# Optimization experiments

Hardware: AMD Instinct MI355X
Metric: run time of the kernel (lower is better)

## Reference

```python
import jax, jax.numpy as jnp
import numpy as np

PAD_TOKEN = -2.0
EPS = 1e-6
NEG_INF = -1.0e9


def _layer_norm(x, gamma, beta):
    mu = jnp.mean(x, axis=-1, keepdims=True)
    var = jnp.mean(jnp.square(x - mu), axis=-1, keepdims=True)
    return (x - mu) * jax.lax.rsqrt(var + EPS) * gamma + beta


def setup_inputs() -> dict:
    key = jax.random.key(0)
    ks = jax.random.split(key, 10)
    B, N, M, D, H, E, O = 128, 32, 384, 256, 8, 32, 256
    S = N + M
    x_pmhc = jax.random.normal(ks[0], (B, S, D), jnp.float32)
    # masks hold raw token values; PAD_TOKEN marks padding positions
    p_len = jax.random.randint(ks[1], (B,), 8, N + 1)
    m_len = jax.random.randint(ks[2], (B,), M // 2, M + 1)
    p_mask = jnp.where(jnp.arange(N)[None, :] < p_len[:, None], 1.0, PAD_TOKEN).astype(jnp.float32)
    m_mask = jnp.where(jnp.arange(M)[None, :] < m_len[:, None], 1.0, PAD_TOKEN).astype(jnp.float32)
    # learned params (keras random_normal init stddev=0.05; random_uniform in [-0.05, 0.05])
    q_proj = 0.05 * jax.random.normal(ks[3], (H, D, E), jnp.float32)
    k_proj = 0.05 * jax.random.normal(ks[4], (H, D, E), jnp.float32)
    v_proj = 0.05 * jax.random.normal(ks[5], (H, D, E), jnp.float32)
    g_proj = jax.random.uniform(ks[6], (H, D, E), jnp.float32, -0.05, 0.05)
    out_w = 0.05 * jax.random.normal(ks[7], (H * E, O), jnp.float32)
    out_b = jnp.zeros((O,), jnp.float32)
    ln1_g = jnp.ones((D,), jnp.float32)
    ln1_b = jnp.zeros((D,), jnp.float32)
    ln2_g = jnp.ones((O,), jnp.float32)
    ln2_b = jnp.zeros((O,), jnp.float32)
    return dict(x_pmhc=x_pmhc, p_mask=p_mask, m_mask=m_mask,
                q_proj=q_proj, k_proj=k_proj, v_proj=v_proj, g_proj=g_proj,
                out_w=out_w, out_b=out_b,
                ln1_g=ln1_g, ln1_b=ln1_b, ln2_g=ln2_g, ln2_b=ln2_b)


def _mask_2d(p, m):
    # p: [B,N] in {0,1}, m: [B,M] in {0,1}
    B, N = p.shape
    M = m.shape[1]
    cross_pm = p[:, :, None] * m[:, None, :]          # [B,N,M]
    cross_mp = m[:, :, None] * p[:, None, :]          # [B,M,N]
    top = jnp.concatenate([jnp.zeros((B, N, N), p.dtype), cross_pm], axis=2)
    bot = jnp.concatenate([cross_mp, jnp.zeros((B, M, M), p.dtype)], axis=2)
    return jnp.concatenate([top, bot], axis=1)        # [B,S,S]


def reference(x_pmhc, p_mask, m_mask, q_proj, k_proj, v_proj, g_proj,
              out_w, out_b, ln1_g, ln1_b, ln2_g, ln2_b):
    H, _, E = q_proj.shape
    B, S, _ = x_pmhc.shape
    scale = 1.0 / jnp.sqrt(jnp.asarray(E, jnp.float32))
    x = _layer_norm(x_pmhc, ln1_g, ln1_b)
    p = jnp.where(p_mask == PAD_TOKEN, 0.0, 1.0)
    m = jnp.where(m_mask == PAD_TOKEN, 0.0, 1.0)
    q = jnp.einsum('bxd,hde->bhxe', x, q_proj)
    k = jnp.einsum('bxd,hde->bhxe', x, k_proj)
    v = jnp.einsum('bxd,hde->bhxe', x, v_proj)
    g = jnp.einsum('bxd,hde->bhxe', x, g_proj)
    att = jnp.einsum('bhxe,bhye->bhxy', q, k) * scale          # [B,H,S,S]
    mask2d = _mask_2d(p, m)                                     # [B,S,S]
    att = jax.nn.softmax(att + ((1.0 - mask2d) * NEG_INF)[:, None], axis=-1)
    att = att * mask2d[:, None]
    out = jnp.einsum('bhxy,bhye->bhxe', att, v)
    out = out * jax.nn.sigmoid(g)
    out = out.transpose(0, 2, 1, 3).reshape(B, S, H * E)
    out = out @ out_w + out_b
    return _layer_norm(out, ln2_g, ln2_b)
```

## Files before the change

kernel.cpp:

```cpp
#include <hip/hip_runtime.h>

typedef unsigned short u16;
typedef __bf16 bf16x8 __attribute__((ext_vector_type(8)));
typedef float f32x4 __attribute__((ext_vector_type(4)));

#define B_    128
#define S_    416
#define NPEP  32
#define MMHC  384
#define D_    256
#define H_    8
#define E_    32
#define O_    256
#define BS_   (B_ * S_)

#define PAD_TOK (-2.0f)
#define SCALE_E 0.17677669529663687f

typedef const __attribute__((address_space(1))) void cg_void;
typedef __attribute__((address_space(3))) void lds_void;

__device__ __forceinline__ float bf2f(u16 u) {
  union { unsigned int i; float f; } x; x.i = ((unsigned int)u) << 16; return x.f;
}
__device__ __forceinline__ u16 f2bf(float f) {
  union { float f; unsigned int i; } x; x.f = f;
  unsigned int i = x.i;
  return (u16)((i + 0x7FFFu + ((i >> 16) & 1u)) >> 16);
}
__device__ __forceinline__ unsigned pk2bf(float lo, float hi) {
  return (unsigned)f2bf(lo) | ((unsigned)f2bf(hi) << 16);
}

__global__ __launch_bounds__(256)
void prep(const float* __restrict__ q, const float* __restrict__ k,
          const float* __restrict__ v, const float* __restrict__ g,
          const float* __restrict__ ow, u16* __restrict__ WT, u16* __restrict__ WoT,
          const float* __restrict__ x, u16* __restrict__ xln,
          const float* __restrict__ gam, const float* __restrict__ bet) {
  const int bx = blockIdx.x, t = threadIdx.x;
  if (bx < 1024) {
    const int col = bx;
    const int p = col >> 8, h = (col >> 5) & 7, e = col & 31;
    const float* src = (p == 0) ? q : (p == 1) ? k : (p == 2) ? v : g;
    WT[col * 256 + t] = f2bf(src[(h * 256 + t) * 32 + e]);
    return;
  }
  if (bx < 1280) {
    const int n = bx - 1024;
    WoT[n * 256 + t] = f2bf(ow[t * 256 + n]);
    return;
  }
  const int w = t >> 6, lane = t & 63;
  const size_t row = (size_t)(bx - 1280) * 4 + w;
  const float4 u = *((const float4*)x + row * 64 + lane);
  const float x0 = u.x, x1 = u.y, x2 = u.z, x3 = u.w;
  float sum = (x0 + x1) + (x2 + x3);
  float ss  = (x0 * x0 + x1 * x1) + (x2 * x2 + x3 * x3);
  #pragma unroll
  for (int off = 32; off; off >>= 1) {
    sum += __shfl_xor(sum, off);
    ss  += __shfl_xor(ss, off);
  }
  const float mean = sum * 0.00390625f;
  float var = ss * 0.00390625f - mean * mean;
  var = fmaxf(var, 0.0f);
  const float rs = rsqrtf(var + 1e-6f);
  const float4 g4 = *((const float4*)gam + lane);
  const float4 b4 = *((const float4*)bet + lane);
  ushort4 r;
  r.x = f2bf((x0 - mean) * rs * g4.x + b4.x);
  r.y = f2bf((x1 - mean) * rs * g4.y + b4.y);
  r.z = f2bf((x2 - mean) * rs * g4.z + b4.z);
  r.w = f2bf((x3 - mean) * rs * g4.w + b4.w);
  *((ushort4*)xln + row * 64 + lane) = r;
}

__global__ __launch_bounds__(256, 4)
void gemm_qkvg(const u16* __restrict__ A, const u16* __restrict__ BT,
               u16* __restrict__ Qh, u16* __restrict__ Kh,
               u16* __restrict__ Vh, u16* __restrict__ Gh) {
  __shared__ __attribute__((aligned(16))) u16 As[128 * 64];
  __shared__ __attribute__((aligned(16))) u16 Bs[128 * 64];
  const int L = blockIdx.x;
  const int m0 = ((L & 7) + 8 * (L >> 6)) * 128;
  const int n0 = ((L >> 3) & 7) * 128;
  const int tid = threadIdx.x;
  const int lane = tid & 63;
  const int w = tid >> 6;
  const int wr = (w >> 1) * 64;
  const int wc = (w & 1) * 64;
  const int mi = lane & 15;
  const int quad = lane >> 4;
  const int rseg = lane >> 3;
  const int gcol = (lane & 7) ^ rseg;
  f32x4 acc[4][4] = {};
  for (int kc = 0; kc < 256; kc += 64) {
    __syncthreads();
    #pragma unroll
    for (int j = 0; j < 4; ++j) {
      const int seg = w * 4 + j;
      const int r = seg * 8 + rseg;
      const u16* ga = &A[(size_t)(m0 + r) * 256 + kc + gcol * 8];
      __builtin_amdgcn_global_load_lds((cg_void*)ga, (lds_void*)&As[seg * 512], 16, 0, 0);
      const u16* gb = &BT[(size_t)(n0 + r) * 256 + kc + gcol * 8];
      __builtin_amdgcn_global_load_lds((cg_void*)gb, (lds_void*)&Bs[seg * 512], 16, 0, 0);
    }
    __syncthreads();
    #pragma unroll
    for (int kt = 0; kt < 2; ++kt) {
      bf16x8 a[4], bb[4];
      #pragma unroll
      for (int i = 0; i < 4; ++i) {
        const int m = wr + i * 16 + mi;
        const int pg = (kt * 4 + quad) ^ (mi & 7);
        a[i] = *(const bf16x8*)&As[m * 64 + pg * 8];
      }
      #pragma unroll
      for (int i = 0; i < 4; ++i) {
        const int n = wc + i * 16 + mi;
        const int pg = (kt * 4 + quad) ^ (mi & 7);
        bb[i] = *(const bf16x8*)&Bs[n * 64 + pg * 8];
      }
      #pragma unroll
      for (int i = 0; i < 4; ++i)
        #pragma unroll
        for (int jn = 0; jn < 4; ++jn)
          acc[i][jn] = __builtin_amdgcn_mfma_f32_16x16x32_bf16(a[i], bb[jn], acc[i][jn], 0, 0, 0);
    }
  }
  u16* dstj[4];
  #pragma unroll
  for (int jn = 0; jn < 4; ++jn) {
    const int colb = n0 + wc + jn * 16;
    const int p = colb >> 8;
    const int h = (colb >> 5) & 7;
    const int e = (colb & 16) + mi;
    u16* bp = (p == 0) ? Qh : (p == 1) ? Kh : (p == 2) ? Vh : Gh;
    dstj[jn] = bp + (size_t)h * BS_ * 32 + e;
  }
  #pragma unroll
  for (int i = 0; i < 4; ++i) {
    const int row = m0 + wr + i * 16 + quad * 4;
    #pragma unroll
    for (int r = 0; r < 4; ++r) {
      #pragma unroll
      for (int jn = 0; jn < 4; ++jn)
        dstj[jn][(size_t)(row + r) * 32] = f2bf(acc[i][jn][r]);
    }
  }
}

__global__ __launch_bounds__(256, 4)
void att_fused(const u16* __restrict__ Qh, const u16* __restrict__ Kh,
               const u16* __restrict__ Vh, const u16* __restrict__ Gh,
               const float* __restrict__ p_mask, const float* __restrict__ m_mask,
               u16* __restrict__ atto) {
  __shared__ __attribute__((aligned(16))) u16 VT[32][392];
  __shared__ __attribute__((aligned(16))) u16 VpT[32][40];
  __shared__ __attribute__((aligned(16))) float pf[32];
  __shared__ __attribute__((aligned(16))) float mfl[384];
  const int bh = blockIdx.x;
  const int b = bh >> 3, h = bh & 7;
  const int t = threadIdx.x;
  const int lane = t & 63, w = t >> 6;
  const int mi = lane & 15, quad = lane >> 4;
  const size_t hb = (size_t)h * BS_ + (size_t)b * S_;

  if (t < 32) pf[t] = (p_mask[b * NPEP + t] == PAD_TOK) ? 0.0f : 1.0f;
  mfl[t] = (m_mask[b * MMHC + t] == PAD_TOK) ? 0.0f : 1.0f;
  if (t < 128) mfl[256 + t] = (m_mask[b * MMHC + 256 + t] == PAD_TOK) ? 0.0f : 1.0f;
  {
    const int y = t >> 3, e0 = (t & 7) * 4;
    const ushort4 u = *(const ushort4*)&Vh[(hb + y) * 32 + e0];
    VpT[e0 + 0][y] = u.x; VpT[e0 + 1][y] = u.y;
    VpT[e0 + 2][y] = u.z; VpT[e0 + 3][y] = u.w;
  }
  #pragma unroll
  for (int i = 0; i < 12; ++i) {
    const int idx = i * 256 + t;
    const int y = idx >> 3, e0 = (idx & 7) * 4;
    const ushort4 u = *(const ushort4*)&Vh[(hb + 32 + y) * 32 + e0];
    VT[e0 + 0][y] = u.x; VT[e0 + 1][y] = u.y;
    VT[e0 + 2][y] = u.z; VT[e0 + 3][y] = u.w;
  }
  __syncthreads();

  const f32x4 fz = {0.0f, 0.0f, 0.0f, 0.0f};
  const int idxA = ((quad & 1) * 2) * 16 + mi;
  const int idxB = idxA + 16;
  const bool hi = quad >= 2;
  union U8 { unsigned u[4]; bf16x8 v; };

  if (w < 2) {
    const bf16x8 aq = *(const bf16x8*)&Qh[(hb + w * 16 + mi) * 32 + quad * 8];
    float lsum = 0.0f;
    f32x4 o0 = fz, o1 = fz;
    #pragma unroll
    for (int ks = 0; ks < 12; ++ks) {
      unsigned pA0, pA1, pB0, pB1;
      {
        const int kt = 2 * ks;
        const bf16x8 bk = *(const bf16x8*)&Kh[(hb + 32 + kt * 16 + mi) * 32 + quad * 8];
        const f32x4 s = __builtin_amdgcn_mfma_f32_16x16x32_bf16(bk, aq, fz, 0, 0, 0);
        const float4 m4 = *(const float4*)&mfl[kt * 16 + quad * 4];
        const float e0 = m4.x * __expf(s[0] * SCALE_E);
        const float e1 = m4.y * __expf(s[1] * SCALE_E);
        const float e2 = m4.z * __expf(s[2] * SCALE_E);
        const float e3 = m4.w * __expf(s[3] * SCALE_E);
        lsum += (e0 + e1) + (e2 + e3);
        pA0 = pk2bf(e0, e1); pA1 = pk2bf(e2, e3);
      }
      {
        const int kt = 2 * ks + 1;
        const bf16x8 bk = *(const bf16x8*)&Kh[(hb + 32 + kt * 16 + mi) * 32 + quad * 8];
        const f32x4 s = __builtin_amdgcn_mfma_f32_16x16x32_bf16(bk, aq, fz, 0, 0, 0);
        const float4 m4 = *(const float4*)&mfl[kt * 16 + quad * 4];
        const float e0 = m4.x * __expf(s[0] * SCALE_E);
        const float e1 = m4.y * __expf(s[1] * SCALE_E);
        const float e2 = m4.z * __expf(s[2] * SCALE_E);
        const float e3 = m4.w * __expf(s[3] * SCALE_E);
        lsum += (e0 + e1) + (e2 + e3);
        pB0 = pk2bf(e0, e1); pB1 = pk2bf(e2, e3);
      }
      const unsigned a00 = __shfl(pA0, idxA), a01 = __shfl(pA1, idxA);
      const unsigned b00 = __shfl(pB0, idxA), b01 = __shfl(pB1, idxA);
      const unsigned a10 = __shfl(pA0, idxB), a11 = __shfl(pA1, idxB);
      const unsigned b10 = __shfl(pB0, idxB), b11 = __shfl(pB1, idxB);
      U8 pf_;
      pf_.u[0] = hi ? b00 : a00;
      pf_.u[1] = hi ? b01 : a01;
      pf_.u[2] = hi ? b10 : a10;
      pf_.u[3] = hi ? b11 : a11;
      const bf16x8 v0 = *(const bf16x8*)&VT[mi][ks * 32 + quad * 8];
      const bf16x8 v1 = *(const bf16x8*)&VT[16 + mi][ks * 32 + quad * 8];
      o0 = __builtin_amdgcn_mfma_f32_16x16x32_bf16(v0, pf_.v, o0, 0, 0, 0);
      o1 = __builtin_amdgcn_mfma_f32_16x16x32_bf16(v1, pf_.v, o1, 0, 0, 0);
    }
    lsum += __shfl_xor(lsum, 16);
    lsum += __shfl_xor(lsum, 32);
    const int prow = w * 16 + mi;
    const float sc = (1.0f / lsum) * pf[prow];
    const ushort4 g0 = *(const ushort4*)&Gh[(hb + prow) * 32 + quad * 4];
    const ushort4 g1 = *(const ushort4*)&Gh[(hb + prow) * 32 + 16 + quad * 4];
    ushort4 r0, r1;
    r0.x = f2bf(o0[0] * sc / (1.0f + __expf(-bf2f(g0.x))));
    r0.y = f2bf(o0[1] * sc / (1.0f + __expf(-bf2f(g0.y))));
    r0.z = f2bf(o0[2] * sc / (1.0f + __expf(-bf2f(g0.z))));
    r0.w = f2bf(o0[3] * sc / (1.0f + __expf(-bf2f(g0.w))));
    r1.x = f2bf(o1[0] * sc / (1.0f + __expf(-bf2f(g1.x))));
    r1.y = f2bf(o1[1] * sc / (1.0f + __expf(-bf2f(g1.y))));
    r1.z = f2bf(o1[2] * sc / (1.0f + __expf(-bf2f(g1.z))));
    r1.w = f2bf(o1[3] * sc / (1.0f + __expf(-bf2f(g1.w))));
    *(ushort4*)&atto[(hb + prow) * 32 + quad * 4] = r0;
    *(ushort4*)&atto[(hb + prow) * 32 + 16 + quad * 4] = r1;
  } else {
    const int wid = w - 2;
    const bf16x8 bk0 = *(const bf16x8*)&Kh[(hb + mi) * 32 + quad * 8];
    const bf16x8 bk1 = *(const bf16x8*)&Kh[(hb + 16 + mi) * 32 + quad * 8];
    const bf16x8 bv0 = *(const bf16x8*)&VpT[mi][quad * 8];
    const bf16x8 bv1 = *(const bf16x8*)&VpT[16 + mi][quad * 8];
    const float4 pfa = *(const float4*)&pf[quad * 4];
    const float4 pfb = *(const float4*)&pf[16 + quad * 4];
    for (int i = 0; i < 12; ++i) {
      const int rloc = (i * 2 + wid) * 16;
      const size_t grow = hb + 32 + rloc + mi;
      const bf16x8 aq = *(const bf16x8*)&Qh[grow * 32 + quad * 8];
      const f32x4 s0 = __builtin_amdgcn_mfma_f32_16x16x32_bf16(bk0, aq, fz, 0, 0, 0);
      const f32x4 s1 = __builtin_amdgcn_mfma_f32_16x16x32_bf16(bk1, aq, fz, 0, 0, 0);
      const float e00 = pfa.x * __expf(s0[0] * SCALE_E);
      const float e01 = pfa.y * __expf(s0[1] * SCALE_E);
      const float e02 = pfa.z * __expf(s0[2] * SCALE_E);
      const float e03 = pfa.w * __expf(s0[3] * SCALE_E);
      const float e10 = pfb.x * __expf(s1[0] * SCALE_E);
      const float e11 = pfb.y * __expf(s1[1] * SCALE_E);
      const float e12 = pfb.z * __expf(s1[2] * SCALE_E);
      const float e13 = pfb.w * __expf(s1[3] * SCALE_E);
      float lsum = ((e00 + e01) + (e02 + e03)) + ((e10 + e11) + (e12 + e13));
      lsum += __shfl_xor(lsum, 16);
      lsum += __shfl_xor(lsum, 32);
      const unsigned pA0 = pk2bf(e00, e01), pA1 = pk2bf(e02, e03);
      const unsigned pB0 = pk2bf(e10, e11), pB1 = pk2bf(e12, e13);
      const unsigned a00 = __shfl(pA0, idxA), a01 = __shfl(pA1, idxA);
      const unsigned b00 = __shfl(pB0, idxA), b01 = __shfl(pB1, idxA);
      const unsigned a10 = __shfl(pA0, idxB), a11 = __shfl(pA1, idxB);
      const unsigned b10 = __shfl(pB0, idxB), b11 = __shfl(pB1, idxB);
      U8 pf_;
      pf_.u[0] = hi ? b00 : a00;
      pf_.u[1] = hi ? b01 : a01;
      pf_.u[2] = hi ? b10 : a10;
      pf_.u[3] = hi ? b11 : a11;
      const f32x4 o0 = __builtin_amdgcn_mfma_f32_16x16x32_bf16(bv0, pf_.v, fz, 0, 0, 0);
      const f32x4 o1 = __builtin_amdgcn_mfma_f32_16x16x32_bf16(bv1, pf_.v, fz, 0, 0, 0);
      const float sc = (1.0f / lsum) * mfl[rloc + mi];
      const ushort4 g0 = *(const ushort4*)&Gh[grow * 32 + quad * 4];
      const ushort4 g1 = *(const ushort4*)&Gh[grow * 32 + 16 + quad * 4];
      ushort4 r0, r1;
      r0.x = f2bf(o0[0] * sc / (1.0f + __expf(-bf2f(g0.x))));
      r0.y = f2bf(o0[1] * sc / (1.0f + __expf(-bf2f(g0.y))));
      r0.z = f2bf(o0[2] * sc / (1.0f + __expf(-bf2f(g0.z))));
      r0.w = f2bf(o0[3] * sc / (1.0f + __expf(-bf2f(g0.w))));
      r1.x = f2bf(o1[0] * sc / (1.0f + __expf(-bf2f(g1.x))));
      r1.y = f2bf(o1[1] * sc / (1.0f + __expf(-bf2f(g1.y))));
      r1.z = f2bf(o1[2] * sc / (1.0f + __expf(-bf2f(g1.z))));
      r1.w = f2bf(o1[3] * sc / (1.0f + __expf(-bf2f(g1.w))));
      *(ushort4*)&atto[grow * 32 + quad * 4] = r0;
      *(ushort4*)&atto[grow * 32 + 16 + quad * 4] = r1;
    }
  }
}

__global__ __launch_bounds__(512, 2)
void gemm2_ln(const u16* __restrict__ A, const u16* __restrict__ BT,
              float* __restrict__ out, const float* __restrict__ bias,
              const float* __restrict__ gam, const float* __restrict__ bet) {
  __shared__ __attribute__((aligned(16))) u16 As[128 * 64];
  __shared__ __attribute__((aligned(16))) u16 Bs[256 * 64];
  __shared__ float rsum[128][4];
  __shared__ float rssq[128][4];
  __shared__ float mean_s[128], rstd_s[128];
  const int m0 = blockIdx.x * 128;
  const int tid = threadIdx.x;
  const int lane = tid & 63;
  const int w = tid >> 6;
  const int wr = (w >> 2) * 64;
  const int wc = (w & 3) * 64;
  const int mi = lane & 15;
  const int quad = lane >> 4;
  const int rseg = lane >> 3;
  const int gcol = (lane & 7) ^ rseg;
  f32x4 acc[4][4] = {};
  for (int kc = 0; kc < 256; kc += 64) {
    __syncthreads();
    #pragma unroll
    for (int j = 0; j < 2; ++j) {
      const int seg = w * 2 + j;
      const int r = seg * 8 + rseg;
      const int c = kc + gcol * 8;
      const u16* ga = &A[((size_t)(c >> 5) * BS_ + (m0 + r)) * 32 + (c & 31)];
      __builtin_amdgcn_global_load_lds((cg_void*)ga, (lds_void*)&As[seg * 512], 16, 0, 0);
    }
    #pragma unroll
    for (int j = 0; j < 4; ++j) {
      const int seg = w * 4 + j;
      const int r = seg * 8 + rseg;
      const u16* gb = &BT[(size_t)r * 256 + kc + gcol * 8];
      __builtin_amdgcn_global_load_lds((cg_void*)gb, (lds_void*)&Bs[seg * 512], 16, 0, 0);
    }
    __syncthreads();
    #pragma unroll
    for (int kt = 0; kt < 2; ++kt) {
      bf16x8 a[4], bb[4];
      #pragma unroll
      for (int i = 0; i < 4; ++i) {
        const int m = wr + i * 16 + mi;
        const int pg = (kt * 4 + quad) ^ (mi & 7);
        a[i] = *(const bf16x8*)&As[m * 64 + pg * 8];
      }
      #pragma unroll
      for (int i = 0; i < 4; ++i) {
        const int n = wc + i * 16 + mi;
        const int pg = (kt * 4 + quad) ^ (mi & 7);
        bb[i] = *(const bf16x8*)&Bs[n * 64 + pg * 8];
      }
      #pragma unroll
      for (int i = 0; i < 4; ++i)
        #pragma unroll
        for (int jn = 0; jn < 4; ++jn)
          acc[i][jn] = __builtin_amdgcn_mfma_f32_16x16x32_bf16(a[i], bb[jn], acc[i][jn], 0, 0, 0);
    }
  }
  float bia[4];
  #pragma unroll
  for (int jn = 0; jn < 4; ++jn) bia[jn] = bias[wc + jn * 16 + mi];
  #pragma unroll
  for (int i = 0; i < 4; ++i) {
    #pragma unroll
    for (int r = 0; r < 4; ++r) {
      float s = 0.0f, qq = 0.0f;
      #pragma unroll
      for (int jn = 0; jn < 4; ++jn) {
        const float v = acc[i][jn][r] + bia[jn];
        s += v; qq += v * v;
      }
      #pragma unroll
      for (int off = 1; off < 16; off <<= 1) {
        s  += __shfl_xor(s, off);
        qq += __shfl_xor(qq, off);
      }
      if (mi == 0) {
        const int rl = wr + i * 16 + quad * 4 + r;
        rsum[rl][w & 3] = s;
        rssq[rl][w & 3] = qq;
      }
    }
  }
  __syncthreads();
  if (tid < 128) {
    const float s = rsum[tid][0] + rsum[tid][1] + rsum[tid][2] + rsum[tid][3];
    const float qq = rssq[tid][0] + rssq[tid][1] + rssq[tid][2] + rssq[tid][3];
    const float mean = s * 0.00390625f;
    float var = qq * 0.00390625f - mean * mean;
    var = fmaxf(var, 0.0f);
    mean_s[tid] = mean;
    rstd_s[tid] = rsqrtf(var + 1e-6f);
  }
  __syncthreads();
  #pragma unroll
  for (int jn = 0; jn < 4; ++jn) {
    const int col = wc + jn * 16 + mi;
    const float gv = gam[col], bv = bet[col];
    #pragma unroll
    for (int i = 0; i < 4; ++i) {
      #pragma unroll
      for (int r = 0; r < 4; ++r) {
        const int rl = wr + i * 16 + quad * 4 + r;
        const float v = acc[i][jn][r] + bia[jn];
        out[(size_t)(m0 + rl) * 256 + col] = (v - mean_s[rl]) * rstd_s[rl] * gv + bv;
      }
    }
  }
}

extern "C" void kernel_launch(void* const* d_in, const int* in_sizes, int n_in,
                              void* d_out, int out_size, void* d_ws, size_t ws_size,
                              hipStream_t stream) {
  const float* x      = (const float*)d_in[0];
  const float* p_mask = (const float*)d_in[1];
  const float* m_mask = (const float*)d_in[2];
  const float* q_proj = (const float*)d_in[3];
  const float* k_proj = (const float*)d_in[4];
  const float* v_proj = (const float*)d_in[5];
  const float* g_proj = (const float*)d_in[6];
  const float* out_w  = (const float*)d_in[7];
  const float* out_b  = (const float*)d_in[8];
  const float* ln1_g  = (const float*)d_in[9];
  const float* ln1_b  = (const float*)d_in[10];
  const float* ln2_g  = (const float*)d_in[11];
  const float* ln2_b  = (const float*)d_in[12];

  char* ws = (char*)d_ws;
  u16* WT   = (u16*)(ws);
  u16* WoT  = (u16*)(ws + 524288);
  u16* attx = (u16*)(ws + 655360);
  u16* Qh   = (u16*)(ws + 27918336);
  u16* Kh   = (u16*)(ws + 55181312);
  u16* Vh   = (u16*)(ws + 82444288);
  u16* Gh   = (u16*)(ws + 109707264);
  float* outp = (float*)d_out;

  hipLaunchKernelGGL(prep, dim3(1280 + BS_ / 4), dim3(256), 0, stream,
                     q_proj, k_proj, v_proj, g_proj, out_w, WT, WoT,
                     x, attx, ln1_g, ln1_b);
  hipLaunchKernelGGL(gemm_qkvg, dim3(8 * (BS_ / 128)), dim3(256), 0, stream,
                     attx, WT, Qh, Kh, Vh, Gh);
  hipLaunchKernelGGL(att_fused, dim3(B_ * H_), dim3(256), 0, stream,
                     Qh, Kh, Vh, Gh, p_mask, m_mask, attx);
  hipLaunchKernelGGL(gemm2_ln, dim3(BS_ / 128), dim3(512), 0, stream,
                     attx, WoT, outp, out_b, ln2_g, ln2_b);
}
```

Before: 256.2 us.

## Fuse QKVG projection into attention kernel, keeping K and V in LDS

Replaces the separate QKVG GEMM and attention kernels with one per-(batch, head) kernel of 512 threads. It computes the head's Q, K, V and G projections from the layer-normed input with weight fragments held in registers, keeping K and V in shared memory. Only Q and G still go to global. This removes the global write and read of K and V and one launch. In exchange, each head block reloads the shared x rows, and more waves split the attention work.

```diff
diff --git a/kernel.cpp b/kernel.cpp
--- a/kernel.cpp
+++ b/kernel.cpp
@@ -76,113 +76,97 @@
   *((ushort4*)xln + row * 64 + lane) = r;
 }
 
-__global__ __launch_bounds__(256, 4)
-void gemm_qkvg(const u16* __restrict__ A, const u16* __restrict__ BT,
-               u16* __restrict__ Qh, u16* __restrict__ Kh,
-               u16* __restrict__ Vh, u16* __restrict__ Gh) {
-  __shared__ __attribute__((aligned(16))) u16 As[128 * 64];
-  __shared__ __attribute__((aligned(16))) u16 Bs[128 * 64];
-  const int L = blockIdx.x;
-  const int m0 = ((L & 7) + 8 * (L >> 6)) * 128;
-  const int n0 = ((L >> 3) & 7) * 128;
-  const int tid = threadIdx.x;
-  const int lane = tid & 63;
-  const int w = tid >> 6;
-  const int wr = (w >> 1) * 64;
-  const int wc = (w & 1) * 64;
-  const int mi = lane & 15;
-  const int quad = lane >> 4;
-  const int rseg = lane >> 3;
-  const int gcol = (lane & 7) ^ rseg;
-  f32x4 acc[4][4] = {};
-  for (int kc = 0; kc < 256; kc += 64) {
-    __syncthreads();
-    #pragma unroll
-    for (int j = 0; j < 4; ++j) {
-      const int seg = w * 4 + j;
-      const int r = seg * 8 + rseg;
-      const u16* ga = &A[(size_t)(m0 + r) * 256 + kc + gcol * 8];
-      __builtin_amdgcn_global_load_lds((cg_void*)ga, (lds_void*)&As[seg * 512], 16, 0, 0);
-      const u16* gb = &BT[(size_t)(n0 + r) * 256 + kc + gcol * 8];
-      __builtin_amdgcn_global_load_lds((cg_void*)gb, (lds_void*)&Bs[seg * 512], 16, 0, 0);
-    }
-    __syncthreads();
-    #pragma unroll
-    for (int kt = 0; kt < 2; ++kt) {
-      bf16x8 a[4], bb[4];
-      #pragma unroll
-      for (int i = 0; i < 4; ++i) {
-        const int m = wr + i * 16 + mi;
-        const int pg = (kt * 4 + quad) ^ (mi & 7);
-        a[i] = *(const bf16x8*)&As[m * 64 + pg * 8];
-      }
-      #pragma unroll
-      for (int i = 0; i < 4; ++i) {
-        const int n = wc + i * 16 + mi;
-        const int pg = (kt * 4 + quad) ^ (mi & 7);
-        bb[i] = *(const bf16x8*)&Bs[n * 64 + pg * 8];
-      }
-      #pragma unroll
-      for (int i = 0; i < 4; ++i)
-        #pragma unroll
-        for (int jn = 0; jn < 4; ++jn)
-          acc[i][jn] = __builtin_amdgcn_mfma_f32_16x16x32_bf16(a[i], bb[jn], acc[i][jn], 0, 0, 0);
-    }
-  }
-  u16* dstj[4];
-  #pragma unroll
-  for (int jn = 0; jn < 4; ++jn) {
-    const int colb = n0 + wc + jn * 16;
-    const int p = colb >> 8;
-    const int h = (colb >> 5) & 7;
-    const int e = (colb & 16) + mi;
-    u16* bp = (p == 0) ? Qh : (p == 1) ? Kh : (p == 2) ? Vh : Gh;
-    dstj[jn] = bp + (size_t)h * BS_ * 32 + e;
-  }
-  #pragma unroll
-  for (int i = 0; i < 4; ++i) {
-    const int row = m0 + wr + i * 16 + quad * 4;
-    #pragma unroll
-    for (int r = 0; r < 4; ++r) {
-      #pragma unroll
-      for (int jn = 0; jn < 4; ++jn)
-        dstj[jn][(size_t)(row + r) * 32] = f2bf(acc[i][jn][r]);
-    }
-  }
-}
-
-__global__ __launch_bounds__(256, 4)
-void att_fused(const u16* __restrict__ Qh, const u16* __restrict__ Kh,
-               const u16* __restrict__ Vh, const u16* __restrict__ Gh,
-               const float* __restrict__ p_mask, const float* __restrict__ m_mask,
-               u16* __restrict__ atto) {
+__global__ __launch_bounds__(512, 2)
+void qkvg_att(const u16* __restrict__ xln, const u16* __restrict__ WT,
+              u16* __restrict__ Qh, u16* __restrict__ Gh,
+              const float* __restrict__ p_mask, const float* __restrict__ m_mask,
+              u16* __restrict__ atto) {
+  __shared__ __attribute__((aligned(16))) u16 xs[32 * 256];
+  __shared__ __attribute__((aligned(16))) u16 Kl[416][40];
   __shared__ __attribute__((aligned(16))) u16 VT[32][392];
   __shared__ __attribute__((aligned(16))) u16 VpT[32][40];
   __shared__ __attribute__((aligned(16))) float pf[32];
   __shared__ __attribute__((aligned(16))) float mfl[384];
-  const int bh = blockIdx.x;
-  const int b = bh >> 3, h = bh & 7;
+  const int bid = blockIdx.x;
+  const int b = (bid & 7) * 16 + (bid >> 6);
+  const int h = (bid >> 3) & 7;
   const int t = threadIdx.x;
   const int lane = t & 63, w = t >> 6;
   const int mi = lane & 15, quad = lane >> 4;
   const size_t hb = (size_t)h * BS_ + (size_t)b * S_;
 
   if (t < 32) pf[t] = (p_mask[b * NPEP + t] == PAD_TOK) ? 0.0f : 1.0f;
-  mfl[t] = (m_mask[b * MMHC + t] == PAD_TOK) ? 0.0f : 1.0f;
-  if (t < 128) mfl[256 + t] = (m_mask[b * MMHC + 256 + t] == PAD_TOK) ? 0.0f : 1.0f;
-  {
-    const int y = t >> 3, e0 = (t & 7) * 4;
-    const ushort4 u = *(const ushort4*)&Vh[(hb + y) * 32 + e0];
-    VpT[e0 + 0][y] = u.x; VpT[e0 + 1][y] = u.y;
-    VpT[e0 + 2][y] = u.z; VpT[e0 + 3][y] = u.w;
-  }
+  if (t < 384) mfl[t] = (m_mask[b * MMHC + t] == PAD_TOK) ? 0.0f : 1.0f;
+
+  const int p = w & 3, mt = w >> 2;
+  bf16x8 wf0[8], wf1[8];
   #pragma unroll
-  for (int i = 0; i < 12; ++i) {
-    const int idx = i * 256 + t;
-    const int y = idx >> 3, e0 = (idx & 7) * 4;
-    const ushort4 u = *(const ushort4*)&Vh[(hb + 32 + y) * 32 + e0];
-    VT[e0 + 0][y] = u.x; VT[e0 + 1][y] = u.y;
-    VT[e0 + 2][y] = u.z; VT[e0 + 3][y] = u.w;
+  for (int kc = 0; kc < 8; ++kc) {
+    wf0[kc] = *(const bf16x8*)&WT[(size_t)(p * 256 + h * 32 + mi) * 256 + kc * 32 + quad * 8];
+    wf1[kc] = *(const bf16x8*)&WT[(size_t)(p * 256 + h * 32 + 16 + mi) * 256 + kc * 32 + quad * 8];
+  }
+
+  const size_t xb = (size_t)b * S_ * 256;
+  for (int c = 0; c < 13; ++c) {
+    __syncthreads();
+    #pragma unroll
+    for (int i = 0; i < 2; ++i) {
+      const int g0 = w * 128 + i * 64;
+      const int gi = g0 + lane;
+      const int r = gi >> 5, sub = gi & 31;
+      const int gs = (sub & 7) ^ (r & 7);
+      const u16* src = &xln[xb + (size_t)(c * 32 + r) * 256 + (sub >> 3) * 64 + gs * 8];
+      __builtin_amdgcn_global_load_lds((cg_void*)src, (lds_void*)&xs[g0 * 8], 16, 0, 0);
+    }
+    __syncthreads();
+    const int m0 = c * 32 + mt * 16;
+    f32x4 a0 = {0.0f, 0.0f, 0.0f, 0.0f};
+    f32x4 a1 = {0.0f, 0.0f, 0.0f, 0.0f};
+    #pragma unroll
+    for (int kc = 0; kc < 8; ++kc) {
+      const int pg = ((kc & 1) * 4 + quad) ^ (mi & 7);
+      const bf16x8 xa = *(const bf16x8*)&xs[(mt * 16 + mi) * 256 + (kc >> 1) * 64 + pg * 8];
+      a0 = __builtin_amdgcn_mfma_f32_16x16x32_bf16(xa, wf0[kc], a0, 0, 0, 0);
+      a1 = __builtin_amdgcn_mfma_f32_16x16x32_bf16(xa, wf1[kc], a1, 0, 0, 0);
+    }
+    if (p == 0) {
+      #pragma unroll
+      for (int r = 0; r < 4; ++r) {
+        const size_t row = hb + m0 + quad * 4 + r;
+        Qh[row * 32 + mi] = f2bf(a0[r]);
+        Qh[row * 32 + 16 + mi] = f2bf(a1[r]);
+      }
+    } else if (p == 1) {
+      #pragma unroll
+      for (int r = 0; r < 4; ++r) {
+        const int row = m0 + quad * 4 + r;
+        Kl[row][mi] = f2bf(a0[r]);
+        Kl[row][16 + mi] = f2bf(a1[r]);
+      }
+    } else if (p == 2) {
+      if (c == 0) {
+        #pragma unroll
+        for (int r = 0; r < 4; ++r) {
+          const int row = m0 + quad * 4 + r;
+          VpT[mi][row] = f2bf(a0[r]);
+          VpT[16 + mi][row] = f2bf(a1[r]);
+        }
+      } else {
+        #pragma unroll
+        for (int r = 0; r < 4; ++r) {
+          const int row = m0 + quad * 4 + r - 32;
+          VT[mi][row] = f2bf(a0[r]);
+          VT[16 + mi][row] = f2bf(a1[r]);
+        }
+      }
+    } else {
+      #pragma unroll
+      for (int r = 0; r < 4; ++r) {
+        const size_t row = hb + m0 + quad * 4 + r;
+        Gh[row * 32 + mi] = f2bf(a0[r]);
+        Gh[row * 32 + 16 + mi] = f2bf(a1[r]);
+      }
+    }
   }
   __syncthreads();
 
@@ -201,7 +185,7 @@
       unsigned pA0, pA1, pB0, pB1;
       {
         const int kt = 2 * ks;
-        const bf16x8 bk = *(const bf16x8*)&Kh[(hb + 32 + kt * 16 + mi) * 32 + quad * 8];
+        const bf16x8 bk = *(const bf16x8*)&Kl[32 + kt * 16 + mi][quad * 8];
         const f32x4 s = __builtin_amdgcn_mfma_f32_16x16x32_bf16(bk, aq, fz, 0, 0, 0);
         const float4 m4 = *(const float4*)&mfl[kt * 16 + quad * 4];
         const float e0 = m4.x * __expf(s[0] * SCALE_E);
@@ -213,7 +197,7 @@
       }
       {
         const int kt = 2 * ks + 1;
-        const bf16x8 bk = *(const bf16x8*)&Kh[(hb + 32 + kt * 16 + mi) * 32 + quad * 8];
+        const bf16x8 bk = *(const bf16x8*)&Kl[32 + kt * 16 + mi][quad * 8];
         const f32x4 s = __builtin_amdgcn_mfma_f32_16x16x32_bf16(bk, aq, fz, 0, 0, 0);
         const float4 m4 = *(const float4*)&mfl[kt * 16 + quad * 4];
         const float e0 = m4.x * __expf(s[0] * SCALE_E);
@@ -256,14 +240,14 @@
     *(ushort4*)&atto[(hb + prow) * 32 + 16 + quad * 4] = r1;
   } else {
     const int wid = w - 2;
-    const bf16x8 bk0 = *(const bf16x8*)&Kh[(hb + mi) * 32 + quad * 8];
-    const bf16x8 bk1 = *(const bf16x8*)&Kh[(hb + 16 + mi) * 32 + quad * 8];
+    const bf16x8 bk0 = *(const bf16x8*)&Kl[mi][quad * 8];
+    const bf16x8 bk1 = *(const bf16x8*)&Kl[16 + mi][quad * 8];
     const bf16x8 bv0 = *(const bf16x8*)&VpT[mi][quad * 8];
     const bf16x8 bv1 = *(const bf16x8*)&VpT[16 + mi][quad * 8];
     const float4 pfa = *(const float4*)&pf[quad * 4];
     const float4 pfb = *(const float4*)&pf[16 + quad * 4];
-    for (int i = 0; i < 12; ++i) {
-      const int rloc = (i * 2 + wid) * 16;
+    for (int i = 0; i < 4; ++i) {
+      const int rloc = (wid * 4 + i) * 16;
       const size_t grow = hb + 32 + rloc + mi;
       const bf16x8 aq = *(const bf16x8*)&Qh[grow * 32 + quad * 8];
       const f32x4 s0 = __builtin_amdgcn_mfma_f32_16x16x32_bf16(bk0, aq, fz, 0, 0, 0);
@@ -442,20 +426,17 @@
   char* ws = (char*)d_ws;
   u16* WT   = (u16*)(ws);
   u16* WoT  = (u16*)(ws + 524288);
-  u16* attx = (u16*)(ws + 655360);
+  u16* xln  = (u16*)(ws + 655360);
   u16* Qh   = (u16*)(ws + 27918336);
-  u16* Kh   = (u16*)(ws + 55181312);
-  u16* Vh   = (u16*)(ws + 82444288);
+  u16* atto = (u16*)(ws + 55181312);
   u16* Gh   = (u16*)(ws + 109707264);
   float* outp = (float*)d_out;
 
   hipLaunchKernelGGL(prep, dim3(1280 + BS_ / 4), dim3(256), 0, stream,
                      q_proj, k_proj, v_proj, g_proj, out_w, WT, WoT,
-                     x, attx, ln1_g, ln1_b);
-  hipLaunchKernelGGL(gemm_qkvg, dim3(8 * (BS_ / 128)), dim3(256), 0, stream,
-                     attx, WT, Qh, Kh, Vh, Gh);
-  hipLaunchKernelGGL(att_fused, dim3(B_ * H_), dim3(256), 0, stream,
-                     Qh, Kh, Vh, Gh, p_mask, m_mask, attx);
+                     x, xln, ln1_g, ln1_b);
+  hipLaunchKernelGGL(qkvg_att, dim3(B_ * H_), dim3(512), 0, stream,
+                     xln, WT, Qh, Gh, p_mask, m_mask, atto);
   hipLaunchKernelGGL(gemm2_ln, dim3(BS_ / 128), dim3(512), 0, stream,
-                     attx, WoT, outp, out_b, ln2_g, ln2_b);
-}
+                     atto, WoT, outp, out_b, ln2_g, ln2_b);
+}
```

Result: faster. 218.4 us (-14.7%).
